# Kernel optimization log

Hardware: AMD Instinct MI355X
Metric: run time of the kernel (lower is better)

The kernel has to match this reference:

```python
import jax, jax.numpy as jnp
import numpy as np

N, C_IN, C_OUT, HID, H = 4096, 512, 512, 128, 4
HEAD_OUT = C_OUT // H  # 128
MID = 4 * C_OUT        # 2048
R = 1.0                # spatial radius r
L = 48                 # sequence window l
NEG = -1e9


def layer_norm(x, g, b, eps=1e-5):
    m = jnp.mean(x, axis=-1, keepdims=True)
    v = jnp.mean(jnp.square(x - m), axis=-1, keepdims=True)
    return (x - m) * jax.lax.rsqrt(v + eps) * g + b


def setup_inputs() -> dict:
    key = jax.random.key(0)
    ks = jax.random.split(key, 16)
    s = lambda fan: 1.0 / np.sqrt(fan)
    return {
        "x":   jax.random.normal(ks[0], (N, C_IN), jnp.float32),
        "pos": jax.random.normal(ks[1], (N, 3), jnp.float32),
        "ori": jax.random.normal(ks[2], (N, 3), jnp.float32),
        "seq": jnp.arange(N, dtype=jnp.int64) if jax.config.jax_enable_x64 else jnp.arange(N, dtype=jnp.int32),
        "batch": jnp.sort(jax.random.randint(ks[3], (N,), 0, 8)),
        "ln1_g": jnp.ones((C_IN,), jnp.float32),
        "ln1_b": jnp.zeros((C_IN,), jnp.float32),
        "ln2_g": jnp.ones((C_OUT,), jnp.float32),
        "ln2_b": jnp.zeros((C_OUT,), jnp.float32),
        "Wq": jax.random.normal(ks[4], (H, C_IN, HID), jnp.float32) * s(C_IN),
        "Wk": jax.random.normal(ks[5], (H, C_IN, HID), jnp.float32) * s(C_IN),
        "Wv": jax.random.normal(ks[6], (H, C_IN, HID), jnp.float32) * s(C_IN),
        "Wo": jax.random.normal(ks[7], (H, HID, HEAD_OUT), jnp.float32) * s(HID),
        "lnm_g": jnp.ones((MID,), jnp.float32),
        "lnm_b": jnp.zeros((MID,), jnp.float32),
        "W1": jax.random.normal(ks[8], (C_OUT, MID), jnp.float32) * s(C_OUT),
        "W2": jax.random.normal(ks[9], (MID, C_OUT), jnp.float32) * s(MID),
    }


def _block(x, pos, ori, seq, batch, ln1_g, ln1_b, ln2_g, ln2_b,
           Wq, Wk, Wv, Wo, lnm_g, lnm_b, W1, W2):
    identity = x
    xn = layer_norm(x, ln1_g, ln1_b)

    # geometry/sequence neighborhood mask: same graph, ||dp||<=r, |ds|<=l
    d2 = jnp.sum(jnp.square(pos[:, None, :] - pos[None, :, :]), axis=-1)  # [N,N]
    ds = jnp.abs(seq[:, None] - seq[None, :])
    mask = (batch[:, None] == batch[None, :]) & (d2 <= R * R) & (ds <= L)

    # all heads at once (original loops over heads; math identical)
    q = jnp.einsum('nc,hcd->hnd', xn, Wq)
    k = jnp.einsum('nc,hcd->hnd', xn, Wk)
    v = jnp.einsum('nc,hcd->hnd', xn, Wv)
    gbias = ori @ ori.T  # geometric orientation bias [N,N]
    scores = jnp.einsum('hnd,hmd->hnm', q, k) / np.sqrt(HID) + gbias[None]
    scores = jnp.where(mask[None], scores, NEG)
    attn = jax.nn.softmax(scores, axis=-1)
    o = jnp.einsum('hnm,hmd->hnd', attn, v)
    o = jnp.einsum('hnd,hde->hne', o, Wo)               # [H,N,HEAD_OUT]
    o = jnp.transpose(o, (1, 0, 2)).reshape(N, C_OUT)   # concat heads

    x = o + identity
    identity = x
    h = layer_norm(x, ln2_g, ln2_b) @ W1
    h = jax.nn.relu(layer_norm(h, lnm_g, lnm_b))
    return h @ W2 + identity


def reference(x, pos, ori, seq, batch, ln1_g, ln1_b, ln2_g, ln2_b,
              Wq, Wk, Wv, Wo, lnm_g, lnm_b, W1, W2):
    return _block(x, pos, ori, seq, batch, ln1_g, ln1_b, ln2_g, ln2_b,
                  Wq, Wk, Wv, Wo, lnm_g, lnm_b, W1, W2)
```

## Files before the change

kernel.cpp:

```cpp
#include <hip/hip_runtime.h>

typedef unsigned short u16;
typedef unsigned int u32;
typedef float f32x4 __attribute__((ext_vector_type(4)));
typedef __bf16 bf16x8 __attribute__((ext_vector_type(8)));

#define N_TOK 4096
#define QKV_LD 1536
#define NH 4
#define HID 128
#define C_OUT 512

__device__ __forceinline__ float b2f(u16 u) { return __uint_as_float(((u32)u) << 16); }
__device__ __forceinline__ u16 f2b(float f) {
  u32 u = __float_as_uint(f);
  u32 r = (u + 0x7fffu + ((u >> 16) & 1u)) >> 16;
  return (u16)r;
}

__device__ __forceinline__ void gload16(const u16* g, u16* l) {
  __builtin_amdgcn_global_load_lds(
      (const __attribute__((address_space(1))) void*)g,
      (__attribute__((address_space(3))) void*)l, 16, 0, 0);
}

__device__ __forceinline__ void tr32(const float* __restrict__ s,
                                     u16* __restrict__ d, int R, int C,
                                     int r0, int c0, u16 (*tile)[33]) {
  const int tx = threadIdx.x & 31, ty = threadIdx.x >> 5;
#pragma unroll
  for (int i = 0; i < 32; i += 8)
    tile[ty + i][tx] = f2b(s[(size_t)(r0 + ty + i) * C + c0 + tx]);
  __syncthreads();
#pragma unroll
  for (int i = 0; i < 32; i += 8)
    d[(size_t)(c0 + ty + i) * R + r0 + tx] = tile[tx][ty + i];
}

__device__ __forceinline__ void ln512_body(
    const float* __restrict__ x, const float* __restrict__ g,
    const float* __restrict__ b, u16* __restrict__ y, int row) {
  const int lane = threadIdx.x & 63;
  const float* xr = x + (size_t)row * 512;
  const int c = lane * 8;
  float4 a0 = *(const float4*)(xr + c);
  float4 a1 = *(const float4*)(xr + c + 4);
  float v[8] = {a0.x, a0.y, a0.z, a0.w, a1.x, a1.y, a1.z, a1.w};
  float s1 = 0.f, s2 = 0.f;
#pragma unroll
  for (int i = 0; i < 8; i++) { s1 += v[i]; s2 += v[i] * v[i]; }
#pragma unroll
  for (int o = 32; o; o >>= 1) { s1 += __shfl_xor(s1, o); s2 += __shfl_xor(s2, o); }
  float mean = s1 * (1.f / 512.f);
  float var = s2 * (1.f / 512.f) - mean * mean;
  float rs = rsqrtf(fmaxf(var, 0.f) + 1e-5f);
  float4 g0 = *(const float4*)(g + c), g1 = *(const float4*)(g + c + 4);
  float4 b0 = *(const float4*)(b + c), b1 = *(const float4*)(b + c + 4);
  float gg[8] = {g0.x, g0.y, g0.z, g0.w, g1.x, g1.y, g1.z, g1.w};
  float bb[8] = {b0.x, b0.y, b0.z, b0.w, b1.x, b1.y, b1.z, b1.w};
  u16 t[8];
#pragma unroll
  for (int i = 0; i < 8; i++) t[i] = f2b((v[i] - mean) * rs * gg[i] + bb[i]);
  *(uint4*)(y + (size_t)row * 512 + c) = *(const uint4*)t;
}

__global__ __launch_bounds__(256) void prep(
    const float* __restrict__ x, const float* __restrict__ ln1g,
    const float* __restrict__ ln1b, u16* __restrict__ xn,
    const float* __restrict__ Wq, const float* __restrict__ Wk,
    const float* __restrict__ Wv, const float* __restrict__ Wo,
    const float* __restrict__ W1,
    u16* __restrict__ Btqkv, u16* __restrict__ Wot, u16* __restrict__ W1t)
{
  __shared__ u16 tile[32][33];
  const int bid = blockIdx.x;
  if (bid < 1024) {
    ln512_body(x, ln1g, ln1b, xn, bid * 4 + (threadIdx.x >> 6));
    return;
  }
  const int idx = bid - 1024;
  const float* s; u16* d; int R, C, r0, c0;
  if (idx < 1024) {
    s = W1; d = W1t; R = 512; C = 2048;
    r0 = (idx >> 6) * 32; c0 = (idx & 63) * 32;
  } else if (idx < 1792) {
    int i = idx - 1024;
    int z = i >> 6, rem = i & 63;
    int which = z >> 2, b = z & 3;
    const float* base = (which == 0) ? Wq : (which == 1) ? Wk : Wv;
    s = base + (size_t)b * 512 * 128;
    d = Btqkv + (size_t)which * 4 * 512 * 128 + (size_t)b * 512 * 128;
    R = 512; C = 128;
    r0 = (rem >> 2) * 32; c0 = (rem & 3) * 32;
  } else {
    int i = idx - 1792;
    int b = i >> 4, rem = i & 15;
    s = Wo + (size_t)b * 128 * 128;
    d = Wot + (size_t)b * 128 * 128;
    R = 128; C = 128;
    r0 = (rem >> 2) * 32; c0 = (rem & 3) * 32;
  }
  tr32(s, d, R, C, r0, c0, tile);
}

__global__ __launch_bounds__(256) void ln512_f32(
    const float* __restrict__ x, const float* __restrict__ g,
    const float* __restrict__ b, u16* __restrict__ y)
{
  ln512_body(x, g, b, y, blockIdx.x * 4 + (threadIdx.x >> 6));
}

__global__ __launch_bounds__(256) void ln2048_bf16_relu(
    const u16* __restrict__ x, const float* __restrict__ g,
    const float* __restrict__ b, u16* __restrict__ y)
{
  const int row = blockIdx.x, tid = threadIdx.x;
  const int c = tid * 8;
  const u16* xr = x + (size_t)row * 2048;
  uint4 u = *(const uint4*)(xr + c);
  u16 e[8]; *(uint4*)e = u;
  float v[8];
#pragma unroll
  for (int i = 0; i < 8; i++) v[i] = b2f(e[i]);
  float s1 = 0.f, s2 = 0.f;
#pragma unroll
  for (int i = 0; i < 8; i++) { s1 += v[i]; s2 += v[i] * v[i]; }
#pragma unroll
  for (int o = 32; o; o >>= 1) { s1 += __shfl_xor(s1, o); s2 += __shfl_xor(s2, o); }
  __shared__ float red[2][4];
  int lane = tid & 63, w = tid >> 6;
  if (lane == 0) { red[0][w] = s1; red[1][w] = s2; }
  __syncthreads();
  s1 = red[0][0] + red[0][1] + red[0][2] + red[0][3];
  s2 = red[1][0] + red[1][1] + red[1][2] + red[1][3];
  float mean = s1 * (1.f / 2048.f);
  float var = s2 * (1.f / 2048.f) - mean * mean;
  float rs = rsqrtf(fmaxf(var, 0.f) + 1e-5f);
  float4 g0 = *(const float4*)(g + c), g1 = *(const float4*)(g + c + 4);
  float4 b0 = *(const float4*)(b + c), b1 = *(const float4*)(b + c + 4);
  float gg[8] = {g0.x, g0.y, g0.z, g0.w, g1.x, g1.y, g1.z, g1.w};
  float bb[8] = {b0.x, b0.y, b0.z, b0.w, b1.x, b1.y, b1.z, b1.w};
  u16 t[8];
#pragma unroll
  for (int i = 0; i < 8; i++)
    t[i] = f2b(fmaxf((v[i] - mean) * rs * gg[i] + bb[i], 0.f));
  *(uint4*)(y + (size_t)row * 2048 + c) = *(const uint4*)t;
}

__global__ __launch_bounds__(512, 4) void gemm128(
    const u16* __restrict__ A, int lda,
    const u16* __restrict__ Bt,
    void* __restrict__ C, int ldc, int outf32,
    const float* __restrict__ res,
    int Kslice, int Ktot, int atomic)
{
  __shared__ u16 As[2][128 * 32];
  __shared__ u16 Bs[2][128 * 32];
  const int bn = blockIdx.x, bm = blockIdx.y;
  const int m0 = bm * 128, n0 = bn * 128;
  const int kbase = blockIdx.z * Kslice;
  const int tid = threadIdx.x;
  const int lane = tid & 63, w = tid >> 6;
  const int wm = (w & 1) * 64;
  const int wn = (w >> 1) * 32;
  const int l16 = lane & 15, quad = lane >> 4;

  const int r_st = tid >> 2;
  const int chunk = (tid & 3) ^ ((tid >> 3) & 3);
  const u16* PA = A + (size_t)(m0 + r_st) * lda + kbase + chunk * 8;
  const u16* PB = Bt + (size_t)(n0 + r_st) * Ktot + kbase + chunk * 8;
  const int wbase = w * 512;

  const int slot8 = (quad ^ ((l16 >> 1) & 3)) * 8;

  f32x4 acc[4][2];
#pragma unroll
  for (int i = 0; i < 4; i++)
#pragma unroll
    for (int j = 0; j < 2; j++) acc[i][j] = (f32x4){0.f, 0.f, 0.f, 0.f};

  gload16(PA, &As[0][wbase]);
  gload16(PB, &Bs[0][wbase]);
  __syncthreads();

  int buf = 0;
  for (int kk = 0; kk < Kslice; kk += 32) {
    if (kk + 32 < Kslice) {
      PA += 32; PB += 32;
      gload16(PA, &As[buf ^ 1][wbase]);
      gload16(PB, &Bs[buf ^ 1][wbase]);
    }
    bf16x8 af[4], bfr[2];
#pragma unroll
    for (int mt = 0; mt < 4; mt++)
      af[mt] = *(const bf16x8*)&As[buf][(wm + mt * 16 + l16) * 32 + slot8];
#pragma unroll
    for (int nt = 0; nt < 2; nt++)
      bfr[nt] = *(const bf16x8*)&Bs[buf][(wn + nt * 16 + l16) * 32 + slot8];
#pragma unroll
    for (int mt = 0; mt < 4; mt++)
#pragma unroll
      for (int nt = 0; nt < 2; nt++)
        acc[mt][nt] = __builtin_amdgcn_mfma_f32_16x16x32_bf16(
            af[mt], bfr[nt], acc[mt][nt], 0, 0, 0);
    __syncthreads();
    buf ^= 1;
  }

#pragma unroll
  for (int mt = 0; mt < 4; mt++)
#pragma unroll
    for (int nt = 0; nt < 2; nt++)
#pragma unroll
      for (int r = 0; r < 4; r++) {
        int gr = m0 + wm + mt * 16 + quad * 4 + r;
        int gc = n0 + wn + nt * 16 + l16;
        size_t off = (size_t)gr * ldc + gc;
        float v = acc[mt][nt][r];
        if (atomic) {
          atomicAdd((float*)C + off, v);
        } else {
          if (res) v += res[off];
          if (outf32) ((float*)C)[off] = v;
          else        ((u16*)C)[off] = f2b(v);
        }
      }
}

#define TQ 16
#define BAND 112
#define KROW 136
#define PROW 120
__global__ __launch_bounds__(256) void attn_mfma(
    const u16* __restrict__ qkv, const float* __restrict__ pos,
    const float* __restrict__ ori, const int* __restrict__ batch,
    const u16* __restrict__ wot, const float* __restrict__ xres,
    float* __restrict__ out,
    const float* __restrict__ W2, u16* __restrict__ W2t)
{
  __shared__ u16 kv[128 * KROW];
  __shared__ u16 qp[TQ * KROW];
  __shared__ float ps[TQ * PROW];
  __shared__ float bpx[BAND], bpy[BAND], bpz[BAND];
  __shared__ float box_[BAND], boy_[BAND], boz_[BAND];
  __shared__ int bb[BAND];

  if (blockIdx.x >= 256) {
    int idx = (blockIdx.x - 256) + blockIdx.y * 256;
    int r0 = (idx >> 4) * 32, c0 = (idx & 15) * 32;
    tr32(W2, W2t, 2048, 512, r0, c0, (u16(*)[33])kv);
    return;
  }

  const int h = blockIdx.y;
  const int bxs = (blockIdx.x & 7) * 32 + (blockIdx.x >> 3);
  const int i0 = bxs * TQ;
  const int j0 = i0 - 48;
  const int tid = threadIdx.x;
  const int lane = tid & 63, w = tid >> 6;
  const int l16 = lane & 15, quad = lane >> 4;

  for (int t = tid; t < BAND; t += 256) {
    int j = j0 + t;
    if (j >= 0 && j < N_TOK) {
      bpx[t] = pos[j * 3 + 0]; bpy[t] = pos[j * 3 + 1]; bpz[t] = pos[j * 3 + 2];
      box_[t] = ori[j * 3 + 0]; boy_[t] = ori[j * 3 + 1]; boz_[t] = ori[j * 3 + 2];
      bb[t] = batch[j];
    } else {
      bpx[t] = bpy[t] = bpz[t] = 0.f;
      box_[t] = boy_[t] = boz_[t] = 0.f;
      bb[t] = -12345;
    }
  }
  for (int idx = tid; idx < BAND * 16; idx += 256) {
    int t = idx >> 4, c8 = (idx & 15) * 8;
    int j = j0 + t;
    int4 val = {0, 0, 0, 0};
    if (j >= 0 && j < N_TOK)
      val = *(const int4*)&qkv[(size_t)j * QKV_LD + 512 + h * HID + c8];
    *(int4*)&kv[t * KROW + c8] = val;
  }
  {
    int q = tid >> 4, c8 = (tid & 15) * 8;
    *(int4*)&qp[q * KROW + c8] =
        *(const int4*)&qkv[(size_t)(i0 + q) * QKV_LD + h * HID + c8];
  }
  __syncthreads();

  {
    bf16x8 af[4];
#pragma unroll
    for (int kc = 0; kc < 4; kc++)
      af[kc] = *(const bf16x8*)&qp[l16 * KROW + kc * 32 + quad * 8];
#pragma unroll
    for (int ti = 0; ti < 2; ti++) {
      int tt = w + ti * 4;
      if (tt < 7) {
        f32x4 acc = (f32x4){0.f, 0.f, 0.f, 0.f};
#pragma unroll
        for (int kc = 0; kc < 4; kc++) {
          bf16x8 bf = *(const bf16x8*)&kv[(tt * 16 + l16) * KROW + kc * 32 + quad * 8];
          acc = __builtin_amdgcn_mfma_f32_16x16x32_bf16(af[kc], bf, acc, 0, 0, 0);
        }
        int t = tt * 16 + l16;
#pragma unroll
        for (int r = 0; r < 4; r++) {
          int q = quad * 4 + r, iq = q + 48;
          int dseq = iq - t;
          bool ok = (bb[t] == bb[iq]) && (dseq <= 48) && (dseq >= -48);
          {
#pragma clang fp contract(off)
            float dx = bpx[iq] - bpx[t], dy = bpy[iq] - bpy[t], dz = bpz[iq] - bpz[t];
            float d2 = dx * dx + dy * dy + dz * dz;
            ok = ok && (d2 <= 1.0f);
          }
          float s = -1e9f;
          if (ok) {
            float gb = box_[iq] * box_[t] + boy_[iq] * boy_[t] + boz_[iq] * boz_[t];
            s = acc[r] * 0.08838834764831845f + gb;
          }
          ps[q * PROW + t] = s;
        }
      }
    }
  }
  __syncthreads();

  for (int idx = tid; idx < BAND * 32; idx += 256) {
    int t = idx >> 5, d4 = (idx & 31) * 4;
    int j = j0 + t;
    uint2 val; val.x = 0; val.y = 0;
    if (j >= 0 && j < N_TOK)
      val = *(const uint2*)&qkv[(size_t)j * QKV_LD + 1024 + h * HID + d4];
    u16 e[4] = {(u16)val.x, (u16)(val.x >> 16), (u16)val.y, (u16)(val.y >> 16)};
#pragma unroll
    for (int jj = 0; jj < 4; jj++) {
      int dd = (jj + tid) & 3;
      kv[(d4 + dd) * KROW + t] = e[dd];
    }
  }
  for (int idx = tid; idx < 128 * 16; idx += 256) {
    int d = idx >> 4, t = BAND + (idx & 15);
    kv[d * KROW + t] = 0;
  }
  {
    int row = tid >> 4, sub = tid & 15;
    float vals[7];
    float m = -1e30f;
#pragma unroll
    for (int i = 0; i < 7; i++) {
      vals[i] = ps[row * PROW + sub + i * 16];
      m = fmaxf(m, vals[i]);
    }
#pragma unroll
    for (int o = 8; o; o >>= 1) m = fmaxf(m, __shfl_xor(m, o));
    float s = 0.f;
#pragma unroll
    for (int i = 0; i < 7; i++) { vals[i] = __expf(vals[i] - m); s += vals[i]; }
#pragma unroll
    for (int o = 8; o; o >>= 1) s += __shfl_xor(s, o);
    float inv = 1.f / s;
#pragma unroll
    for (int i = 0; i < 7; i++)
      qp[row * KROW + sub + i * 16] = f2b(vals[i] * inv);
    qp[row * KROW + BAND + sub] = 0;
  }
  __syncthreads();

  u16 obuf[2][4];
  {
    bf16x8 paf[4];
#pragma unroll
    for (int kc = 0; kc < 4; kc++)
      paf[kc] = *(const bf16x8*)&qp[l16 * KROW + kc * 32 + quad * 8];
#pragma unroll
    for (int ti = 0; ti < 2; ti++) {
      int dt = w + ti * 4;
      f32x4 acc = (f32x4){0.f, 0.f, 0.f, 0.f};
#pragma unroll
      for (int kc = 0; kc < 4; kc++) {
        bf16x8 bf = *(const bf16x8*)&kv[(dt * 16 + l16) * KROW + kc * 32 + quad * 8];
        acc = __builtin_amdgcn_mfma_f32_16x16x32_bf16(paf[kc], bf, acc, 0, 0, 0);
      }
#pragma unroll
      for (int r = 0; r < 4; r++) obuf[ti][r] = f2b(acc[r]);
    }
  }
  __syncthreads();

#pragma unroll
  for (int ti = 0; ti < 2; ti++) {
    int dt = w + ti * 4;
#pragma unroll
    for (int r = 0; r < 4; r++)
      qp[(quad * 4 + r) * KROW + dt * 16 + l16] = obuf[ti][r];
  }
  {
    const u16* wsrc = wot + (size_t)h * HID * HID;
    for (int idx = tid; idx < 128 * 16; idx += 256) {
      int e = idx >> 4, c8 = (idx & 15) * 8;
      *(int4*)&kv[e * KROW + c8] = *(const int4*)&wsrc[e * HID + c8];
    }
  }
  __syncthreads();

  {
    bf16x8 oaf[4];
#pragma unroll
    for (int kc = 0; kc < 4; kc++)
      oaf[kc] = *(const bf16x8*)&qp[l16 * KROW + kc * 32 + quad * 8];
#pragma unroll
    for (int ti = 0; ti < 2; ti++) {
      int et = w + ti * 4;
      f32x4 acc = (f32x4){0.f, 0.f, 0.f, 0.f};
#pragma unroll
      for (int kc = 0; kc < 4; kc++) {
        bf16x8 bf = *(const bf16x8*)&kv[(et * 16 + l16) * KROW + kc * 32 + quad * 8];
        acc = __builtin_amdgcn_mfma_f32_16x16x32_bf16(oaf[kc], bf, acc, 0, 0, 0);
      }
#pragma unroll
      for (int r = 0; r < 4; r++) {
        int q = quad * 4 + r;
        size_t off = (size_t)(i0 + q) * C_OUT + h * HID + et * 16 + l16;
        out[off] = acc[r] + xres[off];
      }
    }
  }
}

#define MB (1048576)
extern "C" void kernel_launch(void* const* d_in, const int* in_sizes, int n_in,
                              void* d_out, int out_size, void* d_ws, size_t ws_size,
                              hipStream_t stream) {
  const float* x    = (const float*)d_in[0];
  const float* pos  = (const float*)d_in[1];
  const float* ori  = (const float*)d_in[2];
  const int*   batch = (const int*)d_in[4];
  const float* ln1g = (const float*)d_in[5];
  const float* ln1b = (const float*)d_in[6];
  const float* ln2g = (const float*)d_in[7];
  const float* ln2b = (const float*)d_in[8];
  const float* Wq = (const float*)d_in[9];
  const float* Wk = (const float*)d_in[10];
  const float* Wv = (const float*)d_in[11];
  const float* Wo = (const float*)d_in[12];
  const float* lnmg = (const float*)d_in[13];
  const float* lnmb = (const float*)d_in[14];
  const float* W1 = (const float*)d_in[15];
  const float* W2 = (const float*)d_in[16];
  float* out = (float*)d_out;

  char* ws = (char*)d_ws;
  u16* xn    = (u16*)(ws + 0);
  u16* x1n   = (u16*)(ws + 0);
  u16* qkv   = (u16*)(ws + 4 * MB);
  u16* h     = (u16*)(ws + 4 * MB);
  u16* Wot   = (u16*)(ws + 16 * MB);
  u16* Btqkv = (u16*)(ws + 20 * MB);
  u16* W2t   = (u16*)(ws + 20 * MB);
  u16* W1t   = (u16*)(ws + 22 * MB);

  prep<<<dim3(2880), 256, 0, stream>>>(x, ln1g, ln1b, xn,
                                       Wq, Wk, Wv, Wo, W1, Btqkv, Wot, W1t);
  gemm128<<<dim3(12, 32, 1), 512, 0, stream>>>(xn, 512, Btqkv, qkv, QKV_LD, 0,
                                               nullptr, 512, 512, 0);
  attn_mfma<<<dim3(512, NH), 256, 0, stream>>>(qkv, pos, ori, batch, Wot, x, out,
                                               W2, W2t);
  ln512_f32<<<dim3(1024), 256, 0, stream>>>(out, ln2g, ln2b, x1n);
  gemm128<<<dim3(16, 32, 1), 512, 0, stream>>>(x1n, 512, W1t, h, 2048, 0,
                                               nullptr, 512, 512, 0);
  ln2048_bf16_relu<<<dim3(4096), 256, 0, stream>>>(h, lnmg, lnmb, h);
  gemm128<<<dim3(4, 32, 2), 512, 0, stream>>>(h, 2048, W2t, out, 512, 1,
                                              nullptr, 1024, 2048, 1);
}
```

Measured before the change: 193.9 us.

## Fuse both LayerNorms into GEMM prologues using epilogue-computed row statistics

Removes the standalone ln512 and ln2048+relu kernels. The attention epilogue and the W1 GEMM epilogue now write per-row partial sums and sums of squares, and the following GEMM reads them to normalize (and ReLU) its A tile while staging it through registers into LDS. This drops two launches and a full read/write pass over the 4096x2048 hidden tensor. In exchange, A loads no longer use the direct global-to-LDS path, and the single-pass variance formula is less numerically robust.

```diff
diff --git a/kernel.cpp b/kernel.cpp
--- a/kernel.cpp
+++ b/kernel.cpp
@@ -103,56 +103,15 @@
   tr32(s, d, R, C, r0, c0, tile);
 }
 
-__global__ __launch_bounds__(256) void ln512_f32(
-    const float* __restrict__ x, const float* __restrict__ g,
-    const float* __restrict__ b, u16* __restrict__ y)
-{
-  ln512_body(x, g, b, y, blockIdx.x * 4 + (threadIdx.x >> 6));
-}
-
-__global__ __launch_bounds__(256) void ln2048_bf16_relu(
-    const u16* __restrict__ x, const float* __restrict__ g,
-    const float* __restrict__ b, u16* __restrict__ y)
-{
-  const int row = blockIdx.x, tid = threadIdx.x;
-  const int c = tid * 8;
-  const u16* xr = x + (size_t)row * 2048;
-  uint4 u = *(const uint4*)(xr + c);
-  u16 e[8]; *(uint4*)e = u;
-  float v[8];
-#pragma unroll
-  for (int i = 0; i < 8; i++) v[i] = b2f(e[i]);
-  float s1 = 0.f, s2 = 0.f;
-#pragma unroll
-  for (int i = 0; i < 8; i++) { s1 += v[i]; s2 += v[i] * v[i]; }
-#pragma unroll
-  for (int o = 32; o; o >>= 1) { s1 += __shfl_xor(s1, o); s2 += __shfl_xor(s2, o); }
-  __shared__ float red[2][4];
-  int lane = tid & 63, w = tid >> 6;
-  if (lane == 0) { red[0][w] = s1; red[1][w] = s2; }
-  __syncthreads();
-  s1 = red[0][0] + red[0][1] + red[0][2] + red[0][3];
-  s2 = red[1][0] + red[1][1] + red[1][2] + red[1][3];
-  float mean = s1 * (1.f / 2048.f);
-  float var = s2 * (1.f / 2048.f) - mean * mean;
-  float rs = rsqrtf(fmaxf(var, 0.f) + 1e-5f);
-  float4 g0 = *(const float4*)(g + c), g1 = *(const float4*)(g + c + 4);
-  float4 b0 = *(const float4*)(b + c), b1 = *(const float4*)(b + c + 4);
-  float gg[8] = {g0.x, g0.y, g0.z, g0.w, g1.x, g1.y, g1.z, g1.w};
-  float bb[8] = {b0.x, b0.y, b0.z, b0.w, b1.x, b1.y, b1.z, b1.w};
-  u16 t[8];
-#pragma unroll
-  for (int i = 0; i < 8; i++)
-    t[i] = f2b(fmaxf((v[i] - mean) * rs * gg[i] + bb[i], 0.f));
-  *(uint4*)(y + (size_t)row * 2048 + c) = *(const uint4*)t;
-}
-
+template <int AMODE>
 __global__ __launch_bounds__(512, 4) void gemm128(
-    const u16* __restrict__ A, int lda,
+    const void* __restrict__ Av, int lda,
     const u16* __restrict__ Bt,
     void* __restrict__ C, int ldc, int outf32,
     const float* __restrict__ res,
-    int Kslice, int Ktot, int atomic)
+    int Kslice, int Ktot, int atomic,
+    const float* __restrict__ lng, const float* __restrict__ lnb,
+    const float* __restrict__ statsIn, float* __restrict__ statsOut)
 {
   __shared__ u16 As[2][128 * 32];
   __shared__ u16 Bs[2][128 * 32];
@@ -166,29 +125,89 @@
   const int l16 = lane & 15, quad = lane >> 4;
 
   const int r_st = tid >> 2;
-  const int chunk = (tid & 3) ^ ((tid >> 3) & 3);
-  const u16* PA = A + (size_t)(m0 + r_st) * lda + kbase + chunk * 8;
-  const u16* PB = Bt + (size_t)(n0 + r_st) * Ktot + kbase + chunk * 8;
+  const int x4 = (tid & 3) ^ ((r_st >> 1) & 3);
   const int wbase = w * 512;
-
   const int slot8 = (quad ^ ((l16 >> 1) & 3)) * 8;
 
+  const u16* PB = Bt + (size_t)(n0 + r_st) * Ktot + kbase + x4 * 8;
+  const u16* PA16 = nullptr; const float* PA32 = nullptr;
+  if constexpr (AMODE == 0)
+    PA16 = (const u16*)Av + (size_t)(m0 + r_st) * lda + kbase + x4 * 8;
+  else if constexpr (AMODE == 1)
+    PA32 = (const float*)Av + (size_t)(m0 + r_st) * lda + kbase + (tid & 3) * 8;
+  else
+    PA16 = (const u16*)Av + (size_t)(m0 + r_st) * lda + kbase + (tid & 3) * 8;
+
+  float mean = 0.f, rs = 0.f;
+  if constexpr (AMODE >= 1) {
+    constexpr int NS = (AMODE == 1) ? 16 : 64;
+    constexpr float RCPC = (AMODE == 1) ? (1.f / 512.f) : (1.f / 2048.f);
+    const float* sp = statsIn + (size_t)(m0 + r_st) * (NS * 2);
+    float s1 = 0.f, s2 = 0.f;
+#pragma unroll 16
+    for (int i = 0; i < NS; i++) { s1 += sp[i * 2]; s2 += sp[i * 2 + 1]; }
+    mean = s1 * RCPC;
+    float var = s2 * RCPC - mean * mean;
+    rs = rsqrtf(fmaxf(var, 0.f) + 1e-5f);
+  }
+
+  float va[8], vg[8], vb[8];
+  auto loadA = [&](int kk) {
+    int c0 = kbase + kk + (tid & 3) * 8;
+    if constexpr (AMODE == 1) {
+      float4 a0 = *(const float4*)(PA32 + kk);
+      float4 a1 = *(const float4*)(PA32 + kk + 4);
+      va[0] = a0.x; va[1] = a0.y; va[2] = a0.z; va[3] = a0.w;
+      va[4] = a1.x; va[5] = a1.y; va[6] = a1.z; va[7] = a1.w;
+    } else {
+      uint4 u = *(const uint4*)(PA16 + kk);
+      u16 e[8]; *(uint4*)e = u;
+#pragma unroll
+      for (int i = 0; i < 8; i++) va[i] = b2f(e[i]);
+    }
+    float4 g0 = *(const float4*)(lng + c0), g1 = *(const float4*)(lng + c0 + 4);
+    float4 b0 = *(const float4*)(lnb + c0), b1 = *(const float4*)(lnb + c0 + 4);
+    vg[0] = g0.x; vg[1] = g0.y; vg[2] = g0.z; vg[3] = g0.w;
+    vg[4] = g1.x; vg[5] = g1.y; vg[6] = g1.z; vg[7] = g1.w;
+    vb[0] = b0.x; vb[1] = b0.y; vb[2] = b0.z; vb[3] = b0.w;
+    vb[4] = b1.x; vb[5] = b1.y; vb[6] = b1.z; vb[7] = b1.w;
+  };
+  auto writeA = [&](int buf) {
+    u16 tmp[8];
+#pragma unroll
+    for (int i = 0; i < 8; i++) {
+      float v = (va[i] - mean) * rs * vg[i] + vb[i];
+      if constexpr (AMODE == 2) v = fmaxf(v, 0.f);
+      tmp[i] = f2b(v);
+    }
+    *(int4*)&As[buf][r_st * 32 + x4 * 8] = *(const int4*)tmp;
+  };
+
   f32x4 acc[4][2];
 #pragma unroll
   for (int i = 0; i < 4; i++)
 #pragma unroll
     for (int j = 0; j < 2; j++) acc[i][j] = (f32x4){0.f, 0.f, 0.f, 0.f};
 
-  gload16(PA, &As[0][wbase]);
+  if constexpr (AMODE == 0) {
+    gload16(PA16, &As[0][wbase]);
+  } else {
+    loadA(0); writeA(0);
+  }
   gload16(PB, &Bs[0][wbase]);
   __syncthreads();
 
   int buf = 0;
   for (int kk = 0; kk < Kslice; kk += 32) {
-    if (kk + 32 < Kslice) {
-      PA += 32; PB += 32;
-      gload16(PA, &As[buf ^ 1][wbase]);
+    bool nxt = kk + 32 < Kslice;
+    if (nxt) {
+      PB += 32;
       gload16(PB, &Bs[buf ^ 1][wbase]);
+      if constexpr (AMODE == 0) {
+        PA16 += 32; gload16(PA16, &As[buf ^ 1][wbase]);
+      } else {
+        loadA(kk + 32);
+      }
     }
     bf16x8 af[4], bfr[2];
 #pragma unroll
@@ -203,12 +222,14 @@
       for (int nt = 0; nt < 2; nt++)
         acc[mt][nt] = __builtin_amdgcn_mfma_f32_16x16x32_bf16(
             af[mt], bfr[nt], acc[mt][nt], 0, 0, 0);
+    if constexpr (AMODE != 0) { if (nxt) writeA(buf ^ 1); }
     __syncthreads();
     buf ^= 1;
   }
 
 #pragma unroll
-  for (int mt = 0; mt < 4; mt++)
+  for (int mt = 0; mt < 4; mt++) {
+    float t1[4] = {0.f, 0.f, 0.f, 0.f}, t2[4] = {0.f, 0.f, 0.f, 0.f};
 #pragma unroll
     for (int nt = 0; nt < 2; nt++)
 #pragma unroll
@@ -224,7 +245,28 @@
           if (outf32) ((float*)C)[off] = v;
           else        ((u16*)C)[off] = f2b(v);
         }
-      }
+        if constexpr (AMODE == 1) { t1[r] += v; t2[r] += v * v; }
+      }
+    if constexpr (AMODE == 1) {
+#pragma unroll
+      for (int r = 0; r < 4; r++) {
+#pragma unroll
+        for (int o = 8; o; o >>= 1) {
+          t1[r] += __shfl_xor(t1[r], o);
+          t2[r] += __shfl_xor(t2[r], o);
+        }
+      }
+      if (l16 == 0) {
+        int slot = bn * 4 + (w >> 1);
+#pragma unroll
+        for (int r = 0; r < 4; r++) {
+          int gr = m0 + wm + mt * 16 + quad * 4 + r;
+          float* sp = statsOut + ((size_t)gr * 64 + slot) * 2;
+          sp[0] = t1[r]; sp[1] = t2[r];
+        }
+      }
+    }
+  }
 }
 
 #define TQ 16
@@ -236,7 +278,8 @@
     const float* __restrict__ ori, const int* __restrict__ batch,
     const u16* __restrict__ wot, const float* __restrict__ xres,
     float* __restrict__ out,
-    const float* __restrict__ W2, u16* __restrict__ W2t)
+    const float* __restrict__ W2, u16* __restrict__ W2t,
+    float* __restrict__ stats1)
 {
   __shared__ u16 kv[128 * KROW];
   __shared__ u16 qp[TQ * KROW];
@@ -409,6 +452,7 @@
 #pragma unroll
     for (int kc = 0; kc < 4; kc++)
       oaf[kc] = *(const bf16x8*)&qp[l16 * KROW + kc * 32 + quad * 8];
+    float s1a[4] = {0.f, 0.f, 0.f, 0.f}, s2a[4] = {0.f, 0.f, 0.f, 0.f};
 #pragma unroll
     for (int ti = 0; ti < 2; ti++) {
       int et = w + ti * 4;
@@ -422,7 +466,25 @@
       for (int r = 0; r < 4; r++) {
         int q = quad * 4 + r;
         size_t off = (size_t)(i0 + q) * C_OUT + h * HID + et * 16 + l16;
-        out[off] = acc[r] + xres[off];
+        float v = acc[r] + xres[off];
+        out[off] = v;
+        s1a[r] += v; s2a[r] += v * v;
+      }
+    }
+#pragma unroll
+    for (int r = 0; r < 4; r++) {
+#pragma unroll
+      for (int o = 8; o; o >>= 1) {
+        s1a[r] += __shfl_xor(s1a[r], o);
+        s2a[r] += __shfl_xor(s2a[r], o);
+      }
+    }
+    if (l16 == 0) {
+#pragma unroll
+      for (int r = 0; r < 4; r++) {
+        int row = i0 + quad * 4 + r;
+        float* sp = stats1 + ((size_t)row * 16 + h * 4 + w) * 2;
+        sp[0] = s1a[r]; sp[1] = s2a[r];
       }
     }
   }
@@ -451,8 +513,9 @@
   float* out = (float*)d_out;
 
   char* ws = (char*)d_ws;
-  u16* xn    = (u16*)(ws + 0);
-  u16* x1n   = (u16*)(ws + 0);
+  u16* xn       = (u16*)(ws + 0);
+  float* stats1 = (float*)(ws + 0);
+  float* stats2 = (float*)(ws + 512 * 1024);
   u16* qkv   = (u16*)(ws + 4 * MB);
   u16* h     = (u16*)(ws + 4 * MB);
   u16* Wot   = (u16*)(ws + 16 * MB);
@@ -462,14 +525,15 @@
 
   prep<<<dim3(2880), 256, 0, stream>>>(x, ln1g, ln1b, xn,
                                        Wq, Wk, Wv, Wo, W1, Btqkv, Wot, W1t);
-  gemm128<<<dim3(12, 32, 1), 512, 0, stream>>>(xn, 512, Btqkv, qkv, QKV_LD, 0,
-                                               nullptr, 512, 512, 0);
+  gemm128<0><<<dim3(12, 32, 1), 512, 0, stream>>>(
+      xn, 512, Btqkv, qkv, QKV_LD, 0, nullptr, 512, 512, 0,
+      nullptr, nullptr, nullptr, nullptr);
   attn_mfma<<<dim3(512, NH), 256, 0, stream>>>(qkv, pos, ori, batch, Wot, x, out,
-                                               W2, W2t);
-  ln512_f32<<<dim3(1024), 256, 0, stream>>>(out, ln2g, ln2b, x1n);
-  gemm128<<<dim3(16, 32, 1), 512, 0, stream>>>(x1n, 512, W1t, h, 2048, 0,
-                                               nullptr, 512, 512, 0);
-  ln2048_bf16_relu<<<dim3(4096), 256, 0, stream>>>(h, lnmg, lnmb, h);
-  gemm128<<<dim3(4, 32, 2), 512, 0, stream>>>(h, 2048, W2t, out, 512, 1,
-                                              nullptr, 1024, 2048, 1);
-}
+                                               W2, W2t, stats1);
+  gemm128<1><<<dim3(16, 32, 1), 512, 0, stream>>>(
+      out, 512, W1t, h, 2048, 0, nullptr, 512, 512, 0,
+      ln2g, ln2b, stats1, stats2);
+  gemm128<2><<<dim3(4, 32, 2), 512, 0, stream>>>(
+      h, 2048, W2t, out, 512, 1, nullptr, 1024, 2048, 1,
+      lnmg, lnmb, stats2, nullptr);
+}
```

Result: slower. 216.0 us (+11.4%).

## Double GEMM K-tile to 64 with XOR swizzle and remap block order

Applied to the files above, without the earlier changes.

The bf16 GEMM kernel now stages 64-wide K slices per iteration instead of 32, with a new 8-way XOR swizzle for LDS rows, so there are half as many barriers per K. Block indices are remapped so that groups of 4 M-tiles share an N column, aiming for better L2 reuse. The block order assumes the grid has gridDim.y of 32 and a width compatible with the id arithmetic, which may not hold for every launch. LDS use doubles, which can lower occupancy.

```diff
diff --git a/kernel.cpp b/kernel.cpp
--- a/kernel.cpp
+++ b/kernel.cpp
@@ -154,9 +154,12 @@
     const float* __restrict__ res,
     int Kslice, int Ktot, int atomic)
 {
-  __shared__ u16 As[2][128 * 32];
-  __shared__ u16 Bs[2][128 * 32];
-  const int bn = blockIdx.x, bm = blockIdx.y;
+  __shared__ u16 As[2][128 * 64];
+  __shared__ u16 Bs[2][128 * 64];
+  const int id = blockIdx.x + gridDim.x * blockIdx.y;
+  const int xr = id & 7, xj = id >> 3;
+  const int bm = xr * 4 + (xj & 3);
+  const int bn = xj >> 2;
   const int m0 = bm * 128, n0 = bn * 128;
   const int kbase = blockIdx.z * Kslice;
   const int tid = threadIdx.x;
@@ -165,13 +168,12 @@
   const int wn = (w >> 1) * 32;
   const int l16 = lane & 15, quad = lane >> 4;
 
-  const int r_st = tid >> 2;
-  const int chunk = (tid & 3) ^ ((tid >> 3) & 3);
-  const u16* PA = A + (size_t)(m0 + r_st) * lda + kbase + chunk * 8;
-  const u16* PB = Bt + (size_t)(n0 + r_st) * Ktot + kbase + chunk * 8;
-  const int wbase = w * 512;
-
-  const int slot8 = (quad ^ ((l16 >> 1) & 3)) * 8;
+  const int sr = tid >> 3;
+  const int sch = (tid & 7) ^ (sr & 7);
+  const u16* PA = A + (size_t)(m0 + sr) * lda + kbase + sch * 8;
+  const u16* PB = Bt + (size_t)(n0 + sr) * Ktot + kbase + sch * 8;
+  const size_t askip = (size_t)64 * lda;
+  const size_t bskip = (size_t)64 * Ktot;
 
   f32x4 acc[4][2];
 #pragma unroll
@@ -179,30 +181,43 @@
 #pragma unroll
     for (int j = 0; j < 2; j++) acc[i][j] = (f32x4){0.f, 0.f, 0.f, 0.f};
 
-  gload16(PA, &As[0][wbase]);
-  gload16(PB, &Bs[0][wbase]);
+  {
+    gload16(PA, &As[0][w * 512]);
+    gload16(PA + askip, &As[0][4096 + w * 512]);
+    gload16(PB, &Bs[0][w * 512]);
+    gload16(PB + bskip, &Bs[0][4096 + w * 512]);
+  }
   __syncthreads();
 
   int buf = 0;
-  for (int kk = 0; kk < Kslice; kk += 32) {
-    if (kk + 32 < Kslice) {
-      PA += 32; PB += 32;
-      gload16(PA, &As[buf ^ 1][wbase]);
-      gload16(PB, &Bs[buf ^ 1][wbase]);
-    }
-    bf16x8 af[4], bfr[2];
-#pragma unroll
-    for (int mt = 0; mt < 4; mt++)
-      af[mt] = *(const bf16x8*)&As[buf][(wm + mt * 16 + l16) * 32 + slot8];
-#pragma unroll
-    for (int nt = 0; nt < 2; nt++)
-      bfr[nt] = *(const bf16x8*)&Bs[buf][(wn + nt * 16 + l16) * 32 + slot8];
-#pragma unroll
-    for (int mt = 0; mt < 4; mt++)
-#pragma unroll
-      for (int nt = 0; nt < 2; nt++)
-        acc[mt][nt] = __builtin_amdgcn_mfma_f32_16x16x32_bf16(
-            af[mt], bfr[nt], acc[mt][nt], 0, 0, 0);
+  for (int kk = 0; kk < Kslice; kk += 64) {
+    if (kk + 64 < Kslice) {
+      PA += 64; PB += 64;
+      gload16(PA, &As[buf ^ 1][w * 512]);
+      gload16(PA + askip, &As[buf ^ 1][4096 + w * 512]);
+      gload16(PB, &Bs[buf ^ 1][w * 512]);
+      gload16(PB + bskip, &Bs[buf ^ 1][4096 + w * 512]);
+    }
+#pragma unroll
+    for (int kc = 0; kc < 2; kc++) {
+      bf16x8 af[4], bfr[2];
+#pragma unroll
+      for (int mt = 0; mt < 4; mt++) {
+        int row = wm + mt * 16 + l16;
+        af[mt] = *(const bf16x8*)&As[buf][row * 64 + (((kc * 4 + quad) ^ (row & 7)) * 8)];
+      }
+#pragma unroll
+      for (int nt = 0; nt < 2; nt++) {
+        int row = wn + nt * 16 + l16;
+        bfr[nt] = *(const bf16x8*)&Bs[buf][row * 64 + (((kc * 4 + quad) ^ (row & 7)) * 8)];
+      }
+#pragma unroll
+      for (int mt = 0; mt < 4; mt++)
+#pragma unroll
+        for (int nt = 0; nt < 2; nt++)
+          acc[mt][nt] = __builtin_amdgcn_mfma_f32_16x16x32_bf16(
+              af[mt], bfr[nt], acc[mt][nt], 0, 0, 0);
+    }
     __syncthreads();
     buf ^= 1;
   }
```

Result: no change. 191.6 us (-1.2%).
